# Kernel tuning notes

Measured on AMD Instinct MI355X. Metric: run time of the kernel, lower is better.

Reference implementation:

```python
import jax, jax.numpy as jnp
import numpy as np

D_MODEL = 256
N_HEADS = 8
D_FFN = 1024
B, N = 4, 1024
HEAD_DIM = D_MODEL // N_HEADS
LN_EPS = 1e-5


def _ln(x, g, b):
    mu = jnp.mean(x, axis=-1, keepdims=True)
    var = jnp.var(x, axis=-1, keepdims=True)
    return (x - mu) * jax.lax.rsqrt(var + LN_EPS) * g + b


def setup_inputs() -> dict:
    key = jax.random.key(0)
    ks = jax.random.split(key, 16)
    s = 0.02
    return {
        "embed": jax.random.normal(ks[0], (B, N, D_MODEL), jnp.float32),
        "refer_bbox": jax.random.uniform(ks[1], (B, N, 4), jnp.float32),
        "dist": jax.random.uniform(ks[2], (B, N, N), jnp.float32),
        "query_pos": jax.random.normal(ks[3], (B, N, D_MODEL), jnp.float32),
        "in_proj_w": jax.random.normal(ks[4], (3 * D_MODEL, D_MODEL), jnp.float32) * s,
        "in_proj_b": jnp.zeros((3 * D_MODEL,), jnp.float32),
        "out_w": jax.random.normal(ks[5], (D_MODEL, D_MODEL), jnp.float32) * s,
        "out_b": jnp.zeros((D_MODEL,), jnp.float32),
        "tau_w": jax.random.normal(ks[6], (N_HEADS, D_MODEL), jnp.float32) * s,
        "tau_b": jax.random.uniform(ks[7], (N_HEADS,), jnp.float32, 0.0, 2.0),
        "w1": jax.random.normal(ks[8], (D_FFN, D_MODEL), jnp.float32) * s,
        "b1": jnp.zeros((D_FFN,), jnp.float32),
        "w2": jax.random.normal(ks[9], (D_MODEL, D_FFN), jnp.float32) * s,
        "b2": jnp.zeros((D_MODEL,), jnp.float32),
        "g1": jnp.ones((D_MODEL,), jnp.float32),
        "beta1": jnp.zeros((D_MODEL,), jnp.float32),
        "g2": jnp.ones((D_MODEL,), jnp.float32),
        "beta2": jnp.zeros((D_MODEL,), jnp.float32),
    }


def reference(embed, refer_bbox, dist, query_pos, in_proj_w, in_proj_b, out_w, out_b,
              tau_w, tau_b, w1, b1, w2, b2, g1, beta1, g2, beta2):
    # tau: (B, N, H) -> (B, H, N); additive bias mask[b,h,i,j] = dist[b,i,j] * tau[b,h,i]
    tau = (embed @ tau_w.T + tau_b).transpose(0, 2, 1)
    bias = dist[:, None, :, :] * tau[..., None]  # (B, H, N, N)

    qk = embed + query_pos  # q = k = embed + pos, v = embed
    wq, wk, wv = jnp.split(in_proj_w, 3, axis=0)
    bq, bk, bv = jnp.split(in_proj_b, 3, axis=0)
    q = (qk @ wq.T + bq).reshape(B, N, N_HEADS, HEAD_DIM)
    k = (qk @ wk.T + bk).reshape(B, N, N_HEADS, HEAD_DIM)
    v = (embed @ wv.T + bv).reshape(B, N, N_HEADS, HEAD_DIM)

    scores = jnp.einsum("bihd,bjhd->bhij", q, k) / np.sqrt(HEAD_DIM) + bias
    attn = jax.nn.softmax(scores, axis=-1)
    ctx = jnp.einsum("bhij,bjhd->bihd", attn, v).reshape(B, N, D_MODEL)
    tgt = ctx @ out_w.T + out_b

    x = _ln(embed + tgt, g1, beta1)
    ffn = jax.nn.relu(x @ w1.T + b1) @ w2.T + b2
    return _ln(x + ffn, g2, beta2)
```

## Files before the change

### kernel.cpp

```cpp
#include <hip/hip_runtime.h>
#include <math.h>

#define D_MODEL 256
#define N_HEADS 8
#define HEAD_DIM 32
#define D_FFN   1024
#define BB      4
#define NN      1024
#define M_TOT   (BB * NN)
#define LN_EPS  1e-5f

#define QSCALE_LOG2E 0.2550348612f
#define LOG2E        1.4426950408889634f

typedef float f32x4 __attribute__((ext_vector_type(4)));
typedef short bf16x8 __attribute__((ext_vector_type(8)));

__device__ __forceinline__ unsigned short f2bf(float f) {
    unsigned int u = __float_as_uint(f);
    unsigned int r = (u + 0x7fffu + ((u >> 16) & 1u)) >> 16;
    return (unsigned short)r;
}
__device__ __forceinline__ ushort4 pack4(float4 v) {
    ushort4 o; o.x = f2bf(v.x); o.y = f2bf(v.y); o.z = f2bf(v.z); o.w = f2bf(v.w);
    return o;
}
__device__ __forceinline__ float fast_exp2(float x) {
#if __has_builtin(__builtin_amdgcn_exp2f)
    return __builtin_amdgcn_exp2f(x);
#else
    return exp2f(x);
#endif
}

__global__ __launch_bounds__(256)
void prep_all_kernel(const float4* __restrict__ e, const float4* __restrict__ qp,
                     ushort4* __restrict__ ebf, ushort4* __restrict__ qkbf,
                     const float4* __restrict__ inw, const float4* __restrict__ outw,
                     const float4* __restrict__ w1, const float4* __restrict__ w2,
                     const float4* __restrict__ tauw,
                     ushort4* __restrict__ o_inw, ushort4* __restrict__ o_outw,
                     ushort4* __restrict__ o_w1, ushort4* __restrict__ o_w2,
                     ushort4* __restrict__ o_taupad) {
    if (blockIdx.x < 1024) {
        int i = blockIdx.x * 256 + threadIdx.x;
        float4 ev = e[i], pv = qp[i];
        ebf[i] = pack4(ev);
        float4 s = make_float4(ev.x + pv.x, ev.y + pv.y, ev.z + pv.z, ev.w + pv.w);
        qkbf[i] = pack4(s);
    } else {
        int i = (blockIdx.x - 1024) * 256 + threadIdx.x;
        if (i < 49152)       o_inw[i] = pack4(inw[i]);
        else if (i < 65536)  o_outw[i - 49152] = pack4(outw[i - 49152]);
        else if (i < 131072) o_w1[i - 65536] = pack4(w1[i - 65536]);
        else if (i < 196608) o_w2[i - 131072] = pack4(w2[i - 131072]);
        else if (i < 200704) {
            int q = i - 196608;
            if (q < 512) o_taupad[q] = pack4(tauw[q]);
            else { ushort4 z = {0, 0, 0, 0}; o_taupad[q] = z; }
        }
    }
}

__global__ __launch_bounds__(256)
void qkv_mfma_kernel(const unsigned short* __restrict__ qk_bf,
                     const unsigned short* __restrict__ emb_bf,
                     const unsigned short* __restrict__ inw_bf,
                     const unsigned short* __restrict__ taupad,
                     const float* __restrict__ in_proj_b, const float* __restrict__ tau_b,
                     unsigned short* __restrict__ qb, unsigned short* __restrict__ kb,
                     unsigned short* __restrict__ vbT, float* __restrict__ taub) {
    const int w    = threadIdx.x >> 6;
    const int lane = threadIdx.x & 63;
    const int l16 = lane & 15, l4 = lane >> 4;
    const int n0 = blockIdx.x * 64;
    const int m0 = blockIdx.y * 64;
    const int wm = (w >> 1) * 32, wn = (w & 1) * 32;

    const unsigned short* A = (blockIdx.x < 8) ? qk_bf : emb_bf;
    const unsigned short* W0 = (n0 < 768) ? &inw_bf[(size_t)(n0 + wn + l16) * D_MODEL]
                                          : &taupad[(size_t)(wn + l16) * D_MODEL];
    const unsigned short* Ar0 = &A[(size_t)(m0 + wm + l16) * D_MODEL];

    f32x4 acc[2][2] = {};
    #pragma unroll
    for (int k0 = 0; k0 < D_MODEL; k0 += 32) {
        bf16x8 a0 = *(const bf16x8*)&Ar0[k0 + l4 * 8];
        bf16x8 a1 = *(const bf16x8*)&Ar0[16 * D_MODEL + k0 + l4 * 8];
        bf16x8 b0 = *(const bf16x8*)&W0[k0 + l4 * 8];
        bf16x8 b1 = *(const bf16x8*)&W0[16 * D_MODEL + k0 + l4 * 8];
        acc[0][0] = __builtin_amdgcn_mfma_f32_16x16x32_bf16(a0, b0, acc[0][0], 0, 0, 0);
        acc[0][1] = __builtin_amdgcn_mfma_f32_16x16x32_bf16(a0, b1, acc[0][1], 0, 0, 0);
        acc[1][0] = __builtin_amdgcn_mfma_f32_16x16x32_bf16(a1, b0, acc[1][0], 0, 0, 0);
        acc[1][1] = __builtin_amdgcn_mfma_f32_16x16x32_bf16(a1, b1, acc[1][1], 0, 0, 0);
    }

    #pragma unroll
    for (int i = 0; i < 2; i++) {
        #pragma unroll
        for (int j = 0; j < 2; j++) {
            #pragma unroll
            for (int r = 0; r < 4; r++) {
                const int m = m0 + wm + i * 16 + l4 * 4 + r;
                const int b = m >> 10, nrow = m & 1023;
                const int c = n0 + wn + j * 16 + l16;
                float v = acc[i][j][r];
                if (c < 256) {
                    v = (v + in_proj_b[c]) * QSCALE_LOG2E;
                    int h = c >> 5, d = c & 31;
                    qb[((size_t)(b * N_HEADS + h) * NN + nrow) * HEAD_DIM + d] = f2bf(v);
                } else if (c < 512) {
                    v += in_proj_b[c];
                    int cc = c - 256; int h = cc >> 5, d = cc & 31;
                    kb[((size_t)(b * N_HEADS + h) * NN + nrow) * HEAD_DIM + d] = f2bf(v);
                } else if (c < 768) {
                    v += in_proj_b[c];
                    int cc = c - 512; int h = cc >> 5, d = cc & 31;
                    vbT[((size_t)(b * N_HEADS + h) * HEAD_DIM + d) * NN + nrow] = f2bf(v);
                } else if (c < 776) {
                    v = (v + tau_b[c - 768]) * LOG2E;
                    taub[(size_t)(b * N_HEADS + (c - 768)) * NN + nrow] = v;
                }
            }
        }
    }
}

__global__ __launch_bounds__(256)
void attn_mfma_kernel(const unsigned short* __restrict__ qb,
                      const unsigned short* __restrict__ kb,
                      const unsigned short* __restrict__ vbT,
                      const float* __restrict__ taub,
                      const float* __restrict__ dist,
                      float* __restrict__ Opart,
                      float* __restrict__ lpart) {
    __shared__ unsigned short Plds[4][16 * 72];
    const int w    = threadIdx.x >> 6;
    const int lane = threadIdx.x & 63;
    const int l16  = lane & 15;
    const int l4   = lane >> 4;
    const int bh = blockIdx.y;
    const int b = bh >> 3;
    const int z = blockIdx.z;
    const int i0 = blockIdx.x * 64 + w * 16;
    const int jbase = z * 256;

    const f32x4 zero = {0.f, 0.f, 0.f, 0.f};
    bf16x8 qf = *(const bf16x8*)&qb[((size_t)bh * NN + i0 + l16) * HEAD_DIM + l4 * 8];

    float tau_r[4];
    const float* drow[4];
    #pragma unroll
    for (int r = 0; r < 4; r++) {
        tau_r[r] = taub[(size_t)bh * NN + i0 + l4 * 4 + r];
        drow[r] = &dist[((size_t)b * NN + i0 + l4 * 4 + r) * NN];
    }

    float l_acc[4] = {0.f, 0.f, 0.f, 0.f};
    f32x4 O0 = zero, O1 = zero;

    unsigned short* pw = &Plds[w][0];
    const unsigned short* kbase = &kb[(size_t)bh * NN * HEAD_DIM];
    const unsigned short* vbase = &vbT[(size_t)bh * HEAD_DIM * NN];

    bf16x8 kf[4];
    float dd[4][4];
    #pragma unroll
    for (int s = 0; s < 4; s++)
        kf[s] = *(const bf16x8*)&kbase[(size_t)(jbase + s * 16 + l16) * HEAD_DIM + l4 * 8];
    #pragma unroll
    for (int s = 0; s < 4; s++)
        #pragma unroll
        for (int r = 0; r < 4; r++)
            dd[s][r] = drow[r][jbase + s * 16 + l16];

    for (int kt = 0; kt < 4; kt++) {
        const int j0 = jbase + kt * 64;
        bf16x8 vf[2][2];
        #pragma unroll
        for (int c = 0; c < 2; c++) {
            vf[c][0] = *(const bf16x8*)&vbase[(size_t)l16 * NN + j0 + c * 32 + l4 * 8];
            vf[c][1] = *(const bf16x8*)&vbase[(size_t)(16 + l16) * NN + j0 + c * 32 + l4 * 8];
        }
        bf16x8 kf_n[4];
        float dd_n[4][4];
        if (kt < 3) {
            const int j1 = j0 + 64;
            #pragma unroll
            for (int s = 0; s < 4; s++)
                kf_n[s] = *(const bf16x8*)&kbase[(size_t)(j1 + s * 16 + l16) * HEAD_DIM + l4 * 8];
            #pragma unroll
            for (int s = 0; s < 4; s++)
                #pragma unroll
                for (int r = 0; r < 4; r++)
                    dd_n[s][r] = drow[r][j1 + s * 16 + l16];
        }

        float parr[4][4];
        #pragma unroll
        for (int s = 0; s < 4; s++) {
            f32x4 S = __builtin_amdgcn_mfma_f32_16x16x32_bf16(qf, kf[s], zero, 0, 0, 0);
            #pragma unroll
            for (int r = 0; r < 4; r++) {
                const float p = fast_exp2(S[r] + dd[s][r] * tau_r[r]);
                parr[s][r] = p;
                l_acc[r] += p;
            }
        }

        #pragma unroll
        for (int s = 0; s < 4; s++)
            #pragma unroll
            for (int r = 0; r < 4; r++)
                pw[(l4 * 4 + r) * 72 + s * 16 + l16] = f2bf(parr[s][r]);
        asm volatile("s_waitcnt lgkmcnt(0)" ::: "memory");
        #pragma unroll
        for (int c = 0; c < 2; c++) {
            bf16x8 pf = *(const bf16x8*)&pw[l16 * 72 + c * 32 + l4 * 8];
            O0 = __builtin_amdgcn_mfma_f32_16x16x32_bf16(pf, vf[c][0], O0, 0, 0, 0);
            O1 = __builtin_amdgcn_mfma_f32_16x16x32_bf16(pf, vf[c][1], O1, 0, 0, 0);
        }

        if (kt < 3) {
            #pragma unroll
            for (int s = 0; s < 4; s++) {
                kf[s] = kf_n[s];
                #pragma unroll
                for (int r = 0; r < 4; r++) dd[s][r] = dd_n[s][r];
            }
        }
    }

    #pragma unroll
    for (int msk = 1; msk < 16; msk <<= 1)
        #pragma unroll
        for (int r = 0; r < 4; r++)
            l_acc[r] += __shfl_xor(l_acc[r], msk, 16);

    #pragma unroll
    for (int r = 0; r < 4; r++) {
        const int i = i0 + l4 * 4 + r;
        float* crow = &Opart[((size_t)(z * 32 + bh) * NN + i) * 32];
        crow[l16]      = O0[r];
        crow[16 + l16] = O1[r];
        if (l16 == 0)
            lpart[(size_t)(z * 32 + bh) * NN + i] = l_acc[r];
    }
}

__global__ __launch_bounds__(512)
void post_kernel(const float* __restrict__ Opart, const float* __restrict__ lpart,
                 const unsigned short* __restrict__ outw,
                 const float* __restrict__ out_b, const float* __restrict__ embed,
                 const float* __restrict__ g1, const float* __restrict__ beta1,
                 const unsigned short* __restrict__ w1, const float* __restrict__ b1,
                 const unsigned short* __restrict__ w2, const float* __restrict__ b2,
                 const float* __restrict__ g2, const float* __restrict__ beta2,
                 float* __restrict__ out) {
    __shared__ float Lh[16][8];
    __shared__ unsigned short cs[16][264];
    __shared__ unsigned short xs[16][264];
    __shared__ unsigned short fs[16][1032];
    __shared__ float sums[8][4][4][2];

    const int tid = threadIdx.x;
    const int w = tid >> 6, lane = tid & 63;
    const int l16 = lane & 15, l4 = lane >> 4;
    const int m0 = blockIdx.x * 16;
    const int b = m0 >> 10;

    if (tid < 128) {
        const int row = tid >> 3, h = tid & 7;
        const int i = (m0 + row) & 1023;
        const int rowA = ((b * 8 + h) << 10) + i;
        float l = 0.f;
        #pragma unroll
        for (int z = 0; z < 4; z++) l += lpart[z * 32768 + rowA];
        Lh[row][h] = 1.0f / l;
    }
    __syncthreads();

    {
        const int row = tid >> 5;
        const int d0 = (tid & 31) * 8;
        const int h = d0 >> 5;
        const int dd = d0 & 31;
        const int i = (m0 + row) & 1023;
        const int rowA = ((b * 8 + h) << 10) + i;
        f32x4 s0 = {0.f, 0.f, 0.f, 0.f}, s1 = {0.f, 0.f, 0.f, 0.f};
        #pragma unroll
        for (int z = 0; z < 4; z++) {
            const float* u = &Opart[((size_t)(z * 32768 + rowA)) * 32 + dd];
            s0 += *(const f32x4*)u;
            s1 += *(const f32x4*)(u + 4);
        }
        const float li = Lh[row][h];
        #pragma unroll
        for (int j = 0; j < 4; j++) {
            cs[row][d0 + j]     = f2bf(s0[j] * li);
            cs[row][d0 + 4 + j] = f2bf(s1[j] * li);
        }
    }
    __syncthreads();

    f32x4 accA[2] = {};
    #pragma unroll
    for (int k0 = 0; k0 < D_MODEL; k0 += 32) {
        bf16x8 a = *(const bf16x8*)&cs[l16][k0 + l4 * 8];
        #pragma unroll
        for (int j = 0; j < 2; j++) {
            const int c = w * 32 + j * 16 + l16;
            bf16x8 bj = *(const bf16x8*)&outw[(size_t)c * D_MODEL + k0 + l4 * 8];
            accA[j] = __builtin_amdgcn_mfma_f32_16x16x32_bf16(a, bj, accA[j], 0, 0, 0);
        }
    }
    float xv[2][4];
    {
        float s_r[4] = {0.f, 0.f, 0.f, 0.f}, q_r[4] = {0.f, 0.f, 0.f, 0.f};
        #pragma unroll
        for (int j = 0; j < 2; j++) {
            const int c = w * 32 + j * 16 + l16;
            const float bs = out_b[c];
            #pragma unroll
            for (int r = 0; r < 4; r++) {
                const int m = m0 + l4 * 4 + r;
                const float t = accA[j][r] + bs + embed[(size_t)m * D_MODEL + c];
                xv[j][r] = t; s_r[r] += t; q_r[r] += t * t;
            }
        }
        #pragma unroll
        for (int msk = 1; msk < 16; msk <<= 1)
            #pragma unroll
            for (int r = 0; r < 4; r++) {
                s_r[r] += __shfl_xor(s_r[r], msk, 16);
                q_r[r] += __shfl_xor(q_r[r], msk, 16);
            }
        if (l16 == 0)
            #pragma unroll
            for (int r = 0; r < 4; r++) {
                sums[w][l4][r][0] = s_r[r];
                sums[w][l4][r][1] = q_r[r];
            }
    }
    __syncthreads();
    #pragma unroll
    for (int r = 0; r < 4; r++) {
        float s = 0.f, q = 0.f;
        #pragma unroll
        for (int ww = 0; ww < 8; ww++) { s += sums[ww][l4][r][0]; q += sums[ww][l4][r][1]; }
        const float mu = s * (1.0f / D_MODEL);
        const float var = q * (1.0f / D_MODEL) - mu * mu;
        const float rstd = rsqrtf(var + LN_EPS);
        #pragma unroll
        for (int j = 0; j < 2; j++) {
            const int c = w * 32 + j * 16 + l16;
            const float ov = (xv[j][r] - mu) * rstd * g1[c] + beta1[c];
            xv[j][r] = ov;
            xs[l4 * 4 + r][c] = f2bf(ov);
        }
    }
    __syncthreads();

    f32x4 accB[8] = {};
    #pragma unroll
    for (int k0 = 0; k0 < D_MODEL; k0 += 32) {
        bf16x8 a = *(const bf16x8*)&xs[l16][k0 + l4 * 8];
        #pragma unroll
        for (int j = 0; j < 8; j++) {
            const int fc = w * 128 + j * 16 + l16;
            bf16x8 bj = *(const bf16x8*)&w1[(size_t)fc * D_MODEL + k0 + l4 * 8];
            accB[j] = __builtin_amdgcn_mfma_f32_16x16x32_bf16(a, bj, accB[j], 0, 0, 0);
        }
    }
    #pragma unroll
    for (int j = 0; j < 8; j++) {
        const int fc = w * 128 + j * 16 + l16;
        const float bs = b1[fc];
        #pragma unroll
        for (int r = 0; r < 4; r++)
            fs[l4 * 4 + r][fc] = f2bf(fmaxf(accB[j][r] + bs, 0.f));
    }
    __syncthreads();

    f32x4 accC[2] = {};
    #pragma unroll 8
    for (int k0 = 0; k0 < D_FFN; k0 += 32) {
        bf16x8 a = *(const bf16x8*)&fs[l16][k0 + l4 * 8];
        #pragma unroll
        for (int j = 0; j < 2; j++) {
            const int c = w * 32 + j * 16 + l16;
            bf16x8 bj = *(const bf16x8*)&w2[(size_t)c * D_FFN + k0 + l4 * 8];
            accC[j] = __builtin_amdgcn_mfma_f32_16x16x32_bf16(a, bj, accC[j], 0, 0, 0);
        }
    }
    float v2[2][4];
    {
        float s_r[4] = {0.f, 0.f, 0.f, 0.f}, q_r[4] = {0.f, 0.f, 0.f, 0.f};
        #pragma unroll
        for (int j = 0; j < 2; j++) {
            const int c = w * 32 + j * 16 + l16;
            const float bs = b2[c];
            #pragma unroll
            for (int r = 0; r < 4; r++) {
                const float t = accC[j][r] + bs + xv[j][r];
                v2[j][r] = t; s_r[r] += t; q_r[r] += t * t;
            }
        }
        #pragma unroll
        for (int msk = 1; msk < 16; msk <<= 1)
            #pragma unroll
            for (int r = 0; r < 4; r++) {
                s_r[r] += __shfl_xor(s_r[r], msk, 16);
                q_r[r] += __shfl_xor(q_r[r], msk, 16);
            }
        if (l16 == 0)
            #pragma unroll
            for (int r = 0; r < 4; r++) {
                sums[w][l4][r][0] = s_r[r];
                sums[w][l4][r][1] = q_r[r];
            }
    }
    __syncthreads();
    #pragma unroll
    for (int r = 0; r < 4; r++) {
        float s = 0.f, q = 0.f;
        #pragma unroll
        for (int ww = 0; ww < 8; ww++) { s += sums[ww][l4][r][0]; q += sums[ww][l4][r][1]; }
        const float mu = s * (1.0f / D_MODEL);
        const float var = q * (1.0f / D_MODEL) - mu * mu;
        const float rstd = rsqrtf(var + LN_EPS);
        const int m = m0 + l4 * 4 + r;
        #pragma unroll
        for (int j = 0; j < 2; j++) {
            const int c = w * 32 + j * 16 + l16;
            out[(size_t)m * D_MODEL + c] = (v2[j][r] - mu) * rstd * g2[c] + beta2[c];
        }
    }
}

extern "C" void kernel_launch(void* const* d_in, const int* in_sizes, int n_in,
                              void* d_out, int out_size, void* d_ws, size_t ws_size,
                              hipStream_t stream) {
    const float* embed     = (const float*)d_in[0];
    const float* dist      = (const float*)d_in[2];
    const float* query_pos = (const float*)d_in[3];
    const float* in_proj_w = (const float*)d_in[4];
    const float* in_proj_b = (const float*)d_in[5];
    const float* out_w     = (const float*)d_in[6];
    const float* out_b     = (const float*)d_in[7];
    const float* tau_w     = (const float*)d_in[8];
    const float* tau_b     = (const float*)d_in[9];
    const float* w1        = (const float*)d_in[10];
    const float* b1        = (const float*)d_in[11];
    const float* w2        = (const float*)d_in[12];
    const float* b2        = (const float*)d_in[13];
    const float* g1        = (const float*)d_in[14];
    const float* beta1     = (const float*)d_in[15];
    const float* g2        = (const float*)d_in[16];
    const float* beta2     = (const float*)d_in[17];
    float* out = (float*)d_out;

    char* ws = (char*)d_ws;
    const size_t MB = 1024 * 1024;
    const size_t KB = 1024;
    unsigned short* emb_bf  = (unsigned short*)(ws);
    unsigned short* qk_bf   = (unsigned short*)(ws + 2 * MB);
    unsigned short* qb      = (unsigned short*)(ws + 4 * MB);
    unsigned short* kb      = (unsigned short*)(ws + 6 * MB);
    unsigned short* vbT     = (unsigned short*)(ws + 8 * MB);
    float*          taub    = (float*)(ws + 10 * MB);
    unsigned short* inw_bf  = (unsigned short*)(ws + 11 * MB);
    unsigned short* outw_bf = (unsigned short*)(ws + 11 * MB + 512 * KB);
    unsigned short* w1_bf   = (unsigned short*)(ws + 12 * MB);
    unsigned short* w2_bf   = (unsigned short*)(ws + 12 * MB + 512 * KB);
    unsigned short* taupad  = (unsigned short*)(ws + 13 * MB);
    float*          Opart   = (float*)(ws + 14 * MB);
    float*          lpart   = (float*)(ws + 30 * MB);

    prep_all_kernel<<<dim3(1808), dim3(256), 0, stream>>>(
        (const float4*)embed, (const float4*)query_pos,
        (ushort4*)emb_bf, (ushort4*)qk_bf,
        (const float4*)in_proj_w, (const float4*)out_w, (const float4*)w1,
        (const float4*)w2, (const float4*)tau_w,
        (ushort4*)inw_bf, (ushort4*)outw_bf, (ushort4*)w1_bf, (ushort4*)w2_bf,
        (ushort4*)taupad);

    qkv_mfma_kernel<<<dim3(13, M_TOT / 64), dim3(256), 0, stream>>>(
        qk_bf, emb_bf, inw_bf, taupad, in_proj_b, tau_b, qb, kb, vbT, taub);

    attn_mfma_kernel<<<dim3(NN / 64, BB * N_HEADS, 4), dim3(256), 0, stream>>>(
        qb, kb, vbT, taub, dist, Opart, lpart);

    post_kernel<<<dim3(M_TOT / 16), dim3(512), 0, stream>>>(
        Opart, lpart, outw_bf, out_b, embed, g1, beta1,
        w1_bf, b1, w2_bf, b2, g2, beta2, out);
}
```

Before: 194.4 us.

## Double post_kernel block to 1024 threads, one 16-column tile per wave

The fused post-attention kernel now runs 16 waves per block instead of 8. Each wave owns one 16-column output tile for the out-projection and FFN2, and splits the K loop into two independent MFMA accumulators to shorten dependency chains. FFN1 work per wave is halved accordingly. This gives more parallelism and latency hiding per 16-row block, at the cost of more register pressure limits under 1024-thread launch bounds, an extra reduction add, and a wider LayerNorm partial-sum reduction.

Result: no change. 191.9 us (-1.3%).

```diff
diff --git a/kernel.cpp b/kernel.cpp
--- a/kernel.cpp
+++ b/kernel.cpp
@@ -248,7 +248,7 @@
     }
 }
 
-__global__ __launch_bounds__(512)
+__global__ __launch_bounds__(1024)
 void post_kernel(const float* __restrict__ Opart, const float* __restrict__ lpart,
                  const unsigned short* __restrict__ outw,
                  const float* __restrict__ out_b, const float* __restrict__ embed,
@@ -261,7 +261,7 @@
     __shared__ unsigned short cs[16][264];
     __shared__ unsigned short xs[16][264];
     __shared__ unsigned short fs[16][1032];
-    __shared__ float sums[8][4][4][2];
+    __shared__ float sums[16][4][4][2];
 
     const int tid = threadIdx.x;
     const int w = tid >> 6, lane = tid & 63;
@@ -280,7 +280,7 @@
     }
     __syncthreads();
 
-    {
+    if (tid < 512) {
         const int row = tid >> 5;
         const int d0 = (tid & 31) * 8;
         const int h = d0 >> 5;
@@ -303,30 +303,30 @@
     }
     __syncthreads();
 
-    f32x4 accA[2] = {};
-    #pragma unroll
-    for (int k0 = 0; k0 < D_MODEL; k0 += 32) {
-        bf16x8 a = *(const bf16x8*)&cs[l16][k0 + l4 * 8];
-        #pragma unroll
-        for (int j = 0; j < 2; j++) {
-            const int c = w * 32 + j * 16 + l16;
-            bf16x8 bj = *(const bf16x8*)&outw[(size_t)c * D_MODEL + k0 + l4 * 8];
-            accA[j] = __builtin_amdgcn_mfma_f32_16x16x32_bf16(a, bj, accA[j], 0, 0, 0);
-        }
-    }
-    float xv[2][4];
+    const int cA = w * 16 + l16;
+    f32x4 a0 = {}, a1 = {};
+    {
+        const unsigned short* wr = &outw[(size_t)cA * D_MODEL];
+        #pragma unroll
+        for (int kk = 0; kk < 4; kk++) {
+            const int k0 = kk * 32, k1 = 128 + kk * 32;
+            bf16x8 x0 = *(const bf16x8*)&cs[l16][k0 + l4 * 8];
+            bf16x8 b0 = *(const bf16x8*)&wr[k0 + l4 * 8];
+            bf16x8 x1 = *(const bf16x8*)&cs[l16][k1 + l4 * 8];
+            bf16x8 b1v = *(const bf16x8*)&wr[k1 + l4 * 8];
+            a0 = __builtin_amdgcn_mfma_f32_16x16x32_bf16(x0, b0, a0, 0, 0, 0);
+            a1 = __builtin_amdgcn_mfma_f32_16x16x32_bf16(x1, b1v, a1, 0, 0, 0);
+        }
+    }
+    float xv[4];
     {
         float s_r[4] = {0.f, 0.f, 0.f, 0.f}, q_r[4] = {0.f, 0.f, 0.f, 0.f};
-        #pragma unroll
-        for (int j = 0; j < 2; j++) {
-            const int c = w * 32 + j * 16 + l16;
-            const float bs = out_b[c];
-            #pragma unroll
-            for (int r = 0; r < 4; r++) {
-                const int m = m0 + l4 * 4 + r;
-                const float t = accA[j][r] + bs + embed[(size_t)m * D_MODEL + c];
-                xv[j][r] = t; s_r[r] += t; q_r[r] += t * t;
-            }
+        const float bs = out_b[cA];
+        #pragma unroll
+        for (int r = 0; r < 4; r++) {
+            const int m = m0 + l4 * 4 + r;
+            const float t = a0[r] + a1[r] + bs + embed[(size_t)m * D_MODEL + cA];
+            xv[r] = t; s_r[r] += t; q_r[r] += t * t;
         }
         #pragma unroll
         for (int msk = 1; msk < 16; msk <<= 1)
@@ -347,34 +347,30 @@
     for (int r = 0; r < 4; r++) {
         float s = 0.f, q = 0.f;
         #pragma unroll
-        for (int ww = 0; ww < 8; ww++) { s += sums[ww][l4][r][0]; q += sums[ww][l4][r][1]; }
+        for (int ww = 0; ww < 16; ww++) { s += sums[ww][l4][r][0]; q += sums[ww][l4][r][1]; }
         const float mu = s * (1.0f / D_MODEL);
         const float var = q * (1.0f / D_MODEL) - mu * mu;
         const float rstd = rsqrtf(var + LN_EPS);
-        #pragma unroll
-        for (int j = 0; j < 2; j++) {
-            const int c = w * 32 + j * 16 + l16;
-            const float ov = (xv[j][r] - mu) * rstd * g1[c] + beta1[c];
-            xv[j][r] = ov;
-            xs[l4 * 4 + r][c] = f2bf(ov);
-        }
-    }
-    __syncthreads();
-
-    f32x4 accB[8] = {};
+        const float ov = (xv[r] - mu) * rstd * g1[cA] + beta1[cA];
+        xv[r] = ov;
+        xs[l4 * 4 + r][cA] = f2bf(ov);
+    }
+    __syncthreads();
+
+    f32x4 accB[4] = {};
     #pragma unroll
     for (int k0 = 0; k0 < D_MODEL; k0 += 32) {
         bf16x8 a = *(const bf16x8*)&xs[l16][k0 + l4 * 8];
         #pragma unroll
-        for (int j = 0; j < 8; j++) {
-            const int fc = w * 128 + j * 16 + l16;
+        for (int j = 0; j < 4; j++) {
+            const int fc = w * 64 + j * 16 + l16;
             bf16x8 bj = *(const bf16x8*)&w1[(size_t)fc * D_MODEL + k0 + l4 * 8];
             accB[j] = __builtin_amdgcn_mfma_f32_16x16x32_bf16(a, bj, accB[j], 0, 0, 0);
         }
     }
     #pragma unroll
-    for (int j = 0; j < 8; j++) {
-        const int fc = w * 128 + j * 16 + l16;
+    for (int j = 0; j < 4; j++) {
+        const int fc = w * 64 + j * 16 + l16;
         const float bs = b1[fc];
         #pragma unroll
         for (int r = 0; r < 4; r++)
@@ -382,29 +378,28 @@
     }
     __syncthreads();
 
-    f32x4 accC[2] = {};
-    #pragma unroll 8
-    for (int k0 = 0; k0 < D_FFN; k0 += 32) {
-        bf16x8 a = *(const bf16x8*)&fs[l16][k0 + l4 * 8];
-        #pragma unroll
-        for (int j = 0; j < 2; j++) {
-            const int c = w * 32 + j * 16 + l16;
-            bf16x8 bj = *(const bf16x8*)&w2[(size_t)c * D_FFN + k0 + l4 * 8];
-            accC[j] = __builtin_amdgcn_mfma_f32_16x16x32_bf16(a, bj, accC[j], 0, 0, 0);
-        }
-    }
-    float v2[2][4];
+    f32x4 c0 = {}, c1 = {};
+    {
+        const unsigned short* wr = &w2[(size_t)cA * D_FFN];
+        #pragma unroll
+        for (int kk = 0; kk < 16; kk++) {
+            const int k0 = kk * 32, k1 = 512 + kk * 32;
+            bf16x8 f0 = *(const bf16x8*)&fs[l16][k0 + l4 * 8];
+            bf16x8 b0 = *(const bf16x8*)&wr[k0 + l4 * 8];
+            bf16x8 f1 = *(const bf16x8*)&fs[l16][k1 + l4 * 8];
+            bf16x8 b1v = *(const bf16x8*)&wr[k1 + l4 * 8];
+            c0 = __builtin_amdgcn_mfma_f32_16x16x32_bf16(f0, b0, c0, 0, 0, 0);
+            c1 = __builtin_amdgcn_mfma_f32_16x16x32_bf16(f1, b1v, c1, 0, 0, 0);
+        }
+    }
+    float v2[4];
     {
         float s_r[4] = {0.f, 0.f, 0.f, 0.f}, q_r[4] = {0.f, 0.f, 0.f, 0.f};
-        #pragma unroll
-        for (int j = 0; j < 2; j++) {
-            const int c = w * 32 + j * 16 + l16;
-            const float bs = b2[c];
-            #pragma unroll
-            for (int r = 0; r < 4; r++) {
-                const float t = accC[j][r] + bs + xv[j][r];
-                v2[j][r] = t; s_r[r] += t; q_r[r] += t * t;
-            }
+        const float bs = b2[cA];
+        #pragma unroll
+        for (int r = 0; r < 4; r++) {
+            const float t = c0[r] + c1[r] + bs + xv[r];
+            v2[r] = t; s_r[r] += t; q_r[r] += t * t;
         }
         #pragma unroll
         for (int msk = 1; msk < 16; msk <<= 1)
@@ -425,16 +420,12 @@
     for (int r = 0; r < 4; r++) {
         float s = 0.f, q = 0.f;
         #pragma unroll
-        for (int ww = 0; ww < 8; ww++) { s += sums[ww][l4][r][0]; q += sums[ww][l4][r][1]; }
+        for (int ww = 0; ww < 16; ww++) { s += sums[ww][l4][r][0]; q += sums[ww][l4][r][1]; }
         const float mu = s * (1.0f / D_MODEL);
         const float var = q * (1.0f / D_MODEL) - mu * mu;
         const float rstd = rsqrtf(var + LN_EPS);
         const int m = m0 + l4 * 4 + r;
-        #pragma unroll
-        for (int j = 0; j < 2; j++) {
-            const int c = w * 32 + j * 16 + l16;
-            out[(size_t)m * D_MODEL + c] = (v2[j][r] - mu) * rstd * g2[c] + beta2[c];
-        }
+        out[(size_t)m * D_MODEL + cA] = (v2[r] - mu) * rstd * g2[cA] + beta2[cA];
     }
 }
 
@@ -491,7 +482,7 @@
     attn_mfma_kernel<<<dim3(NN / 64, BB * N_HEADS, 4), dim3(256), 0, stream>>>(
         qb, kb, vbT, taub, dist, Opart, lpart);
 
-    post_kernel<<<dim3(M_TOT / 16), dim3(512), 0, stream>>>(
+    post_kernel<<<dim3(M_TOT / 16), dim3(1024), 0, stream>>>(
         Opart, lpart, outw_bf, out_b, embed, g1, beta1,
         w1_bf, b1, w2_bf, b2, g2, beta2, out);
 }
```
